# Optimization experiments

Hardware: AMD Instinct MI355X
Metric: run time of the kernel (lower is better)

## Reference

```python
import jax, jax.numpy as jnp
import numpy as np

B, T, D, C, L, H = 8192, 128, 1, 1, 1, 64


def _mlp(x, w1, b1, w2, b2):
    # Linear -> Softplus -> Linear
    return jax.nn.softplus(x @ w1 + b1) @ w2 + b2


def setup_inputs() -> dict:
    key = jax.random.key(0)
    ks = jax.random.split(key, 32)
    s = 0.1

    def w(k, shape):
        return jax.random.normal(k, shape, jnp.float32) * s

    p = {}
    p["xs"] = jax.random.normal(ks[0], (T, B, D), jnp.float32)
    p["ts"] = jnp.arange(T, dtype=jnp.float32)
    p["noise_std"] = jnp.float32(5.0)
    p["eps0"] = jax.random.normal(ks[1], (B, L), jnp.float32)
    p["dW_std"] = jax.random.normal(ks[2], (T - 1, B, L), jnp.float32)
    # encoder: data -> hidden -> context
    p["ew1"] = w(ks[3], (D, H)); p["eb1"] = w(ks[4], (H,))
    p["ew2"] = w(ks[5], (H, C)); p["eb2"] = w(ks[6], (C,))
    # qz0_net: context -> 2*latent
    p["qw"] = w(ks[7], (C, 2 * L)); p["qb"] = w(ks[8], (2 * L,))
    # f_net: latent+context -> hidden -> latent
    p["fw1"] = w(ks[9], (L + C, H)); p["fb1"] = w(ks[10], (H,))
    p["fw2"] = w(ks[11], (H, L)); p["fb2"] = w(ks[12], (L,))
    # h_net: latent -> hidden -> latent
    p["hw1"] = w(ks[13], (L, H)); p["hb1"] = w(ks[14], (H,))
    p["hw2"] = w(ks[15], (H, L)); p["hb2"] = w(ks[16], (L,))
    # g_nets: L independent 1 -> hidden -> 1 -> sigmoid nets, stacked on leading L axis
    p["gw1"] = w(ks[17], (L, H)); p["gb1"] = w(ks[18], (L, H))
    p["gw2"] = w(ks[19], (L, H)); p["gb2"] = w(ks[20], (L,))
    # projector: latent -> hidden -> data
    p["pw1"] = w(ks[21], (L, H)); p["pb1"] = w(ks[22], (H,))
    p["pw2"] = w(ks[23], (H, D)); p["pb2"] = w(ks[24], (D,))
    p["pz0_mean"] = jnp.zeros((1, L), jnp.float32)
    p["pz0_logstd"] = jnp.zeros((1, L), jnp.float32)
    return p


def reference(xs, ts, noise_std, eps0, dW_std,
              ew1, eb1, ew2, eb2, qw, qb,
              fw1, fb1, fw2, fb2, hw1, hb1, hw2, hb2,
              gw1, gb1, gw2, gb2, pw1, pb1, pw2, pb2,
              pz0_mean, pz0_logstd):
    Tn = ts.shape[0]
    # ctx = flip(encoder(flip(xs)))  (encoder is pointwise in time)
    ctx = jnp.flip(_mlp(jnp.flip(xs, axis=0), ew1, eb1, ew2, eb2), axis=0)  # [T,B,C]
    qz = ctx[0] @ qw + qb
    qm, qls = jnp.split(qz, 2, axis=1)  # [B,L] each
    z0 = qm + jnp.exp(qls) * eps0

    def g_fn(z):  # per-coordinate diagonal diffusion nets
        hid = jax.nn.softplus(z[:, :, None] * gw1[None] + gb1[None])  # [B,L,H]
        return jax.nn.sigmoid(jnp.einsum('blh,lh->bl', hid, gw2) + gb2)

    def step(z, inp):
        k, dwk = inp
        t = ts[k]
        dt = ts[k + 1] - ts[k]
        idx = jnp.minimum(jnp.searchsorted(ts, t, side='right'), Tn - 1)
        c = jnp.take(ctx, idx, axis=0)  # [B,C]
        fv = _mlp(jnp.concatenate([z, c], axis=1), fw1, fb1, fw2, fb2)
        hv = _mlp(z, hw1, hb1, hw2, hb2)
        gv = g_fn(z)
        u = (fv - hv) / gv
        lr = 0.5 * jnp.sum(u * u, axis=1) * dt  # logqp path increment [B]
        z_next = z + fv * dt + gv * dwk * jnp.sqrt(dt)  # Euler-Maruyama
        return z_next, (z_next, lr)

    _, (ztail, log_ratio) = jax.lax.scan(step, z0, (jnp.arange(Tn - 1), dW_std))
    zs = jnp.concatenate([z0[None], ztail], axis=0)  # [T,B,L]
    _xs = _mlp(zs, pw1, pb1, pw2, pb2)  # [T,B,D]
    lp = -0.5 * ((xs - _xs) / noise_std) ** 2 - jnp.log(noise_std) - 0.5 * jnp.log(2 * jnp.pi)
    log_pxs = lp.sum(axis=(0, 2)).mean()
    kl = (pz0_logstd - qls) + (jnp.exp(2 * qls) + (qm - pz0_mean) ** 2) / (2 * jnp.exp(2 * pz0_logstd)) - 0.5
    logqp0 = kl.sum(axis=1).mean()
    logqp_path = log_ratio.sum(axis=0).mean()
    return (log_pxs, logqp0 + logqp_path)
```

## Files before the change

kernel.cpp:

```cpp
#include <hip/hip_runtime.h>
#include <math.h>


#define B_SZ 8192
#define T_SZ 128
#define NBLK 32

#define NT1 2049
#define NT2 1025
#define NEE 1024
#define NENT (NT1 + NT2 + NEE)

#define MT_FLOATS (8 * (NT1 + NT2))
#define ET2G_OFF  MT_FLOATS
#define TABG_FLOATS (MT_FLOATS + 2048)
#define T2_BASE4 (2 * NT1)

#define NXI 1024
#define XSF 64.0f
#define XOF 512.0f

#if __has_builtin(__builtin_amdgcn_rcpf)
#define RCPF(x) __builtin_amdgcn_rcpf(x)
#else
#define RCPF(x) (1.0f / (x))
#endif
#if __has_builtin(__builtin_amdgcn_sqrtf)
#define SQRTF(x) __builtin_amdgcn_sqrtf(x)
#else
#define SQRTF(x) sqrtf(x)
#endif

__device__ __forceinline__ float sp_precise(float a) {
  return fmaxf(a, 0.0f) + log1pf(expf(-fabsf(a)));
}
__device__ __forceinline__ float wsum64(float v) {
  #pragma unroll
  for (int m = 1; m <= 32; m <<= 1) v += __shfl_xor(v, m);
  return v;
}

__global__ __launch_bounds__(256) void build_tabs(
    const float* __restrict__ ew1, const float* __restrict__ eb1,
    const float* __restrict__ ew2, const float* __restrict__ eb2,
    const float* __restrict__ fw1, const float* __restrict__ fb1,
    const float* __restrict__ fw2, const float* __restrict__ fb2,
    const float* __restrict__ hw1, const float* __restrict__ hb1,
    const float* __restrict__ hw2, const float* __restrict__ hb2,
    const float* __restrict__ gw1, const float* __restrict__ gb1,
    const float* __restrict__ gw2, const float* __restrict__ gb2,
    const float* __restrict__ pw1, const float* __restrict__ pb1,
    const float* __restrict__ pw2, const float* __restrict__ pb2,
    float* __restrict__ tabs, int* __restrict__ ctr)
{
  const int gtid = blockIdx.x * 256 + threadIdx.x;
  if (gtid == 0) *ctr = 0;
  const int ent  = gtid >> 6;
  const int lane = threadIdx.x & 63;
  if (ent >= NENT) return;

  if (ent < NT1 + NT2) {
    const bool t1 = ent < NT1;
    const int  i  = t1 ? ent : (ent - NT1);
    const float z = t1 ? (-128.0f + (float)i * 0.125f)
                       : (-8192.0f + (float)i * 16.0f);
    const int base4 = (t1 ? 0 : T2_BASE4) + 2 * i;

    const float az = fmaf(z, fw1[lane], fb1[lane]);
    const float wc = fw1[64 + lane], w2 = fw2[lane];
    float s0 = sp_precise(fmaf(-3.0f, wc, az)) * w2;
    float s1 = sp_precise(fmaf(-1.0f, wc, az)) * w2;
    float s2 = sp_precise(fmaf( 1.0f, wc, az)) * w2;
    float s3 = sp_precise(fmaf( 3.0f, wc, az)) * w2;
    float sh = sp_precise(fmaf(z, hw1[lane], hb1[lane])) * hw2[lane];
    float sg = sp_precise(fmaf(z, gw1[lane], gb1[lane])) * gw2[lane];
    float sp = sp_precise(fmaf(z, pw1[lane], pb1[lane])) * pw2[lane];
    s0 = wsum64(s0); s1 = wsum64(s1); s2 = wsum64(s2); s3 = wsum64(s3);
    sh = wsum64(sh); sg = wsum64(sg); sp = wsum64(sp);
    if (lane == 0) {
      const float fb = fb2[0];
      ((float4*)tabs)[base4]     = make_float4(s0 + fb, s1 + fb, s2 + fb, s3 + fb);
      ((float4*)tabs)[base4 + 1] = make_float4(
          sh + hb2[0],
          1.0f / (1.0f + expf(-(sg + gb2[0]))),
          sp + pb2[0], 0.0f);
    }
  } else {
    const int i = ent - (NT1 + NT2);
    const float x0 = -8.0f + (float)i * (1.0f / 64.0f);
    const float x1 = x0 + (1.0f / 64.0f);
    const float w = ew1[lane], bb = eb1[lane], w2 = ew2[lane];
    float s0 = sp_precise(fmaf(x0, w, bb)) * w2;
    float s1 = sp_precise(fmaf(x1, w, bb)) * w2;
    s0 = wsum64(s0); s1 = wsum64(s1);
    if (lane == 0) {
      const float eb = eb2[0];
      ((float2*)(tabs + ET2G_OFF))[i] = make_float2(s0 + eb, s1 + eb);
    }
  }
}

__global__ __launch_bounds__(256) void ctx_pre(
    const float* __restrict__ xs, const float* __restrict__ tabs,
    float* __restrict__ ctx)
{
  const int i = blockIdx.x * 256 + threadIdx.x;
  const float2* et2 = (const float2*)(tabs + ET2G_OFF);
  const float s = fmaf(xs[i], XSF, XOF);
  const float sc = fminf(fmaxf(s, 0.0f), (float)(NXI - 1));
  const int ii = (int)sc;
  const float fr = s - (float)ii;
  const float2 e = et2[ii];
  ctx[i] = fmaf(fr, e.y - e.x, e.x);
}

__global__ __launch_bounds__(256) void sde_scan(
    const float* __restrict__ xs, const float* __restrict__ ts,
    const float* __restrict__ noise_std, const float* __restrict__ eps0,
    const float* __restrict__ dW, const float* __restrict__ ctx,
    const float* __restrict__ qw,  const float* __restrict__ qb,
    const float* __restrict__ fw1, const float* __restrict__ fb1,
    const float* __restrict__ fw2, const float* __restrict__ fb2,
    const float* __restrict__ hw1, const float* __restrict__ hb1,
    const float* __restrict__ hw2, const float* __restrict__ hb2,
    const float* __restrict__ gw1, const float* __restrict__ gb1,
    const float* __restrict__ gw2, const float* __restrict__ gb2,
    const float* __restrict__ pw1, const float* __restrict__ pb1,
    const float* __restrict__ pw2, const float* __restrict__ pb2,
    const float* __restrict__ pz0_mean, const float* __restrict__ pz0_logstd,
    const float* __restrict__ tabsrc,
    int* __restrict__ ctr, float* __restrict__ partA, float* __restrict__ partB,
    float* __restrict__ out)
{
  __shared__ __align__(16) float tab[MT_FLOATS];
  __shared__ float la[256], lb[256];
  __shared__ int lastflag;

  const int tid = threadIdx.x;
  const int b   = blockIdx.x * 256 + tid;

  {
    const float4* s4 = (const float4*)tabsrc;
    float4* d4 = (float4*)tab;
    for (int i = tid; i < MT_FLOATS / 4; i += 256) d4[i] = s4[i];
  }
  __syncthreads();

  const float4* tab4 = (const float4*)tab;

  const float fb2s = fb2[0], hb2s = hb2[0], gb2s = gb2[0], pb2s = pb2[0];
  const float qw0 = qw[0], qw1 = qw[1], qb0 = qb[0], qb1 = qb[1];
  const float ns = noise_std[0];
  const float inv_ns = 1.0f / ns;
  const float nh_i2 = -0.5f * inv_ns * inv_ns;
  const float pm = pz0_mean[0], pls = pz0_logstd[0];

  auto lagr = [&](float c) {
    const float c2 = c * c;
    const float p1 = c2 - 1.0f, p3 = c2 - 9.0f;
    return make_float4(p1 * (c - 3.0f) * (-1.0f / 48.0f),
                       p3 * (c - 1.0f) * ( 1.0f / 16.0f),
                       p3 * (c + 1.0f) * (-1.0f / 16.0f),
                       p1 * (c + 3.0f) * ( 1.0f / 48.0f));
  };
  auto hgp_exact = [&](float z, float& hv, float& gv, float& pv) {
    float sh = 0.f, sg = 0.f, sp = 0.f;
    for (int j = 0; j < 64; ++j) {
      sh = fmaf(sp_precise(fmaf(z, hw1[j], hb1[j])), hw2[j], sh);
      sg = fmaf(sp_precise(fmaf(z, gw1[j], gb1[j])), gw2[j], sg);
      sp = fmaf(sp_precise(fmaf(z, pw1[j], pb1[j])), pw2[j], sp);
    }
    hv = sh + hb2s;
    gv = 1.0f / (1.0f + expf(-(sg + gb2s)));
    pv = sp + pb2s;
  };
  auto f_exact = [&](float z, float c) {
    float s = 0.f;
    for (int j = 0; j < 64; ++j)
      s = fmaf(sp_precise(fmaf(z, fw1[j], fmaf(c, fw1[64 + j], fb1[j]))), fw2[j], s);
    return s + fb2s;
  };

  auto zidx = [&](float z, int& base4, float& frac, bool& inr) {
    const float s1 = fmaf(z, 8.0f, 1024.0f);
    const float s2 = fmaf(z, 0.0625f, 512.0f);
    const bool t1 = (s1 >= 0.0f) && (s1 <= 2048.0f);
    const bool t2 = (s2 >= 0.0f) && (s2 <= 1024.0f);
    inr = t1 || t2;
    const float sf = t1 ? s1 : fminf(fmaxf(s2, 0.0f), 1024.0f);
    const int fi = min((int)sf, t1 ? (NT1 - 2) : (NT2 - 2));
    base4 = (t1 ? 0 : T2_BASE4) + 2 * fi;
    frac = sf - (float)fi;
  };

  const float x0 = xs[b];
  float x1 = xs[B_SZ + b];
  float x2 = xs[2 * B_SZ + b];
  const float c0v = ctx[b];
  float c_cur = ctx[B_SZ + b];
  float c_nxt = ctx[2 * B_SZ + b];
  const float qm  = fmaf(c0v, qw0, qb0);
  const float qls = fmaf(c0v, qw1, qb1);
  float z = fmaf(__expf(qls), eps0[b], qm);
  const float dqm = qm - pm;
  const float kl = (pls - qls)
                 + (__expf(2.0f * qls) + dqm * dqm) * (0.5f * __expf(-2.0f * pls))
                 - 0.5f;

  bool zin; int zb4; float zfr;
  float4 q0a, q0b, q1a, q1b;
  float hv, gv, pv;
  zidx(z, zb4, zfr, zin);
  q0a = tab4[zb4]; q0b = tab4[zb4 + 1]; q1a = tab4[zb4 + 2]; q1b = tab4[zb4 + 3];
  if (zin) {
    hv = fmaf(zfr, q1b.x - q0b.x, q0b.x);
    gv = fmaf(zfr, q1b.y - q0b.y, q0b.y);
    pv = fmaf(zfr, q1b.z - q0b.z, q0b.z);
  } else {
    hgp_exact(z, hv, gv, pv);
  }
  float lp_sum; { const float d = x0 - pv; lp_sum = nh_i2 * d * d; }
  float lr_sum = 0.0f;
  float dw_cur = dW[b];
  float dw_n1  = dW[B_SZ + b];
  float4 L = lagr(c_cur);
  bool cin = fabsf(c_cur) <= 3.0f;

  for (int k = 0; k < T_SZ - 1; ++k) {
    const int   i3    = (k + 3 < T_SZ) ? (k + 3) : (T_SZ - 1);
    const float x3    = xs[i3 * B_SZ + b];
    const float c3    = ctx[i3 * B_SZ + b];
    const float dw_n2 = (k + 2 < T_SZ - 1) ? dW[(k + 2) * B_SZ + b] : 0.0f;
    const float dt    = ts[k + 1] - ts[k];
    const float sq    = SQRTF(dt);

    float fv;
    if (zin && cin) {
      const float n0 = fmaf(zfr, q1a.x - q0a.x, q0a.x);
      const float n1 = fmaf(zfr, q1a.y - q0a.y, q0a.y);
      const float n2 = fmaf(zfr, q1a.z - q0a.z, q0a.z);
      const float n3 = fmaf(zfr, q1a.w - q0a.w, q0a.w);
      fv = n0 * L.x + n1 * L.y + n2 * L.z + n3 * L.w;
    } else {
      fv = f_exact(z, c_cur);
    }

    const float gvs = fmaxf(gv, 1e-6f);
    const float uu = (fv - hv) * RCPF(gvs);
    lr_sum = fmaf((0.5f * dt) * uu, uu, lr_sum);
    z = fmaf(gvs * dw_cur, sq, fmaf(fv, dt, z));

    zidx(z, zb4, zfr, zin);
    q0a = tab4[zb4]; q0b = tab4[zb4 + 1]; q1a = tab4[zb4 + 2]; q1b = tab4[zb4 + 3];
    if (zin) {
      hv = fmaf(zfr, q1b.x - q0b.x, q0b.x);
      gv = fmaf(zfr, q1b.y - q0b.y, q0b.y);
      pv = fmaf(zfr, q1b.z - q0b.z, q0b.z);
    } else {
      hgp_exact(z, hv, gv, pv);
    }

    const float d = x1 - pv;
    lp_sum = fmaf(nh_i2 * d, d, lp_sum);

    c_cur = c_nxt; L = lagr(c_cur); cin = fabsf(c_cur) <= 3.0f;
    c_nxt = c3;
    x1 = x2; x2 = x3;
    dw_cur = dw_n1; dw_n1 = dw_n2;
  }

  la[tid] = lp_sum; lb[tid] = kl + lr_sum;
  __syncthreads();
  for (int s = 128; s > 0; s >>= 1) {
    if (tid < s) { la[tid] += la[tid + s]; lb[tid] += lb[tid + s]; }
    __syncthreads();
  }
  if (tid == 0) {
    partA[blockIdx.x] = la[0]; partB[blockIdx.x] = lb[0];
    __threadfence();
    lastflag = (atomicAdd(ctr, 1) == NBLK - 1) ? 1 : 0;
  }
  __syncthreads();
  if (lastflag) {
    __threadfence();
    la[tid] = (tid < NBLK) ? partA[tid] : 0.0f;
    lb[tid] = (tid < NBLK) ? partB[tid] : 0.0f;
    __syncthreads();
    for (int s = 128; s > 0; s >>= 1) {
      if (tid < s) { la[tid] += la[tid + s]; lb[tid] += lb[tid + s]; }
      __syncthreads();
    }
    if (tid == 0) {
      out[0] = la[0] / (float)B_SZ
             + (float)T_SZ * (-__logf(ns) - 0.9189385332046727f);
      out[1] = lb[0] / (float)B_SZ;
    }
  }
}

extern "C" void kernel_launch(void* const* d_in, const int* in_sizes, int n_in,
                              void* d_out, int out_size, void* d_ws, size_t ws_size,
                              hipStream_t stream) {
  const float* xs        = (const float*)d_in[0];
  const float* ts        = (const float*)d_in[1];
  const float* noise_std = (const float*)d_in[2];
  const float* eps0      = (const float*)d_in[3];
  const float* dW        = (const float*)d_in[4];
  const float* ew1 = (const float*)d_in[5];
  const float* eb1 = (const float*)d_in[6];
  const float* ew2 = (const float*)d_in[7];
  const float* eb2 = (const float*)d_in[8];
  const float* qw  = (const float*)d_in[9];
  const float* qb  = (const float*)d_in[10];
  const float* fw1 = (const float*)d_in[11];
  const float* fb1 = (const float*)d_in[12];
  const float* fw2 = (const float*)d_in[13];
  const float* fb2 = (const float*)d_in[14];
  const float* hw1 = (const float*)d_in[15];
  const float* hb1 = (const float*)d_in[16];
  const float* hw2 = (const float*)d_in[17];
  const float* hb2 = (const float*)d_in[18];
  const float* gw1 = (const float*)d_in[19];
  const float* gb1 = (const float*)d_in[20];
  const float* gw2 = (const float*)d_in[21];
  const float* gb2 = (const float*)d_in[22];
  const float* pw1 = (const float*)d_in[23];
  const float* pb1 = (const float*)d_in[24];
  const float* pw2 = (const float*)d_in[25];
  const float* pb2 = (const float*)d_in[26];
  const float* pz0_mean   = (const float*)d_in[27];
  const float* pz0_logstd = (const float*)d_in[28];
  float* out = (float*)d_out;

  float* tabs  = (float*)d_ws;
  int*   ctr   = (int*)(tabs + TABG_FLOATS);
  float* partA = tabs + TABG_FLOATS + 4;
  float* partB = partA + NBLK;
  float* ctxb  = tabs + TABG_FLOATS + 72;

  build_tabs<<<(NENT * 64 + 255) / 256, 256, 0, stream>>>(
      ew1, eb1, ew2, eb2, fw1, fb1, fw2, fb2,
      hw1, hb1, hw2, hb2, gw1, gb1, gw2, gb2,
      pw1, pb1, pw2, pb2, tabs, ctr);

  ctx_pre<<<(T_SZ * B_SZ) / 256, 256, 0, stream>>>(xs, tabs, ctxb);

  sde_scan<<<NBLK, 256, 0, stream>>>(
      xs, ts, noise_std, eps0, dW, ctxb, qw, qb,
      fw1, fb1, fw2, fb2, hw1, hb1, hw2, hb2,
      gw1, gb1, gw2, gb2, pw1, pb1, pw2, pb2,
      pz0_mean, pz0_logstd, tabs, ctr, partA, partB, out);
}
```

Measured before the change: 73.85 us.

## Shrink z lookup table, pad entries to three float4s, deepen prefetch to four steps

Halves the resolution of the fine z table (step 0.25 instead of 0.125) so it holds half as many entries, and gives each entry a stride of three float4 instead of two, with the third slot zero-filled. The time loop is manually unrolled by four and uses a four-deep rotating register buffer for xs, ctx and dW loads, which hides global load latency across more steps. The coarser table lowers interpolation accuracy for f/h/g/p, and the padded stride adds table memory and raises the chance of gather cache misses.

```diff
diff --git a/kernel.cpp b/kernel.cpp
--- a/kernel.cpp
+++ b/kernel.cpp
@@ -6,15 +6,16 @@
 #define T_SZ 128
 #define NBLK 32
 
-#define NT1 2049
+#define NT1 1025
 #define NT2 1025
 #define NEE 1024
 #define NENT (NT1 + NT2 + NEE)
 
-#define MT_FLOATS (8 * (NT1 + NT2))
+#define ENT_F4 3
+#define MT_FLOATS (4 * ENT_F4 * (NT1 + NT2))
+#define T2_BASE4 (ENT_F4 * NT1)
 #define ET2G_OFF  MT_FLOATS
 #define TABG_FLOATS (MT_FLOATS + 2048)
-#define T2_BASE4 (2 * NT1)
 
 #define NXI 1024
 #define XSF 64.0f
@@ -62,9 +63,9 @@
   if (ent < NT1 + NT2) {
     const bool t1 = ent < NT1;
     const int  i  = t1 ? ent : (ent - NT1);
-    const float z = t1 ? (-128.0f + (float)i * 0.125f)
+    const float z = t1 ? (-128.0f + (float)i * 0.25f)
                        : (-8192.0f + (float)i * 16.0f);
-    const int base4 = (t1 ? 0 : T2_BASE4) + 2 * i;
+    const int base4 = (t1 ? 0 : T2_BASE4) + ENT_F4 * i;
 
     const float az = fmaf(z, fw1[lane], fb1[lane]);
     const float wc = fw1[64 + lane], w2 = fw2[lane];
@@ -84,6 +85,7 @@
           sh + hb2[0],
           1.0f / (1.0f + expf(-(sg + gb2[0]))),
           sp + pb2[0], 0.0f);
+      ((float4*)tabs)[base4 + 2] = make_float4(0.f, 0.f, 0.f, 0.f);
     }
   } else {
     const int i = ent - (NT1 + NT2);
@@ -163,42 +165,37 @@
                        p3 * (c + 1.0f) * (-1.0f / 16.0f),
                        p1 * (c + 3.0f) * ( 1.0f / 48.0f));
   };
-  auto hgp_exact = [&](float z, float& hv, float& gv, float& pv) {
+  auto hgp_exact = [&](float z_, float& hv_, float& gv_, float& pv_) {
     float sh = 0.f, sg = 0.f, sp = 0.f;
     for (int j = 0; j < 64; ++j) {
-      sh = fmaf(sp_precise(fmaf(z, hw1[j], hb1[j])), hw2[j], sh);
-      sg = fmaf(sp_precise(fmaf(z, gw1[j], gb1[j])), gw2[j], sg);
-      sp = fmaf(sp_precise(fmaf(z, pw1[j], pb1[j])), pw2[j], sp);
-    }
-    hv = sh + hb2s;
-    gv = 1.0f / (1.0f + expf(-(sg + gb2s)));
-    pv = sp + pb2s;
+      sh = fmaf(sp_precise(fmaf(z_, hw1[j], hb1[j])), hw2[j], sh);
+      sg = fmaf(sp_precise(fmaf(z_, gw1[j], gb1[j])), gw2[j], sg);
+      sp = fmaf(sp_precise(fmaf(z_, pw1[j], pb1[j])), pw2[j], sp);
+    }
+    hv_ = sh + hb2s;
+    gv_ = 1.0f / (1.0f + expf(-(sg + gb2s)));
+    pv_ = sp + pb2s;
   };
-  auto f_exact = [&](float z, float c) {
+  auto f_exact = [&](float z_, float c_) {
     float s = 0.f;
     for (int j = 0; j < 64; ++j)
-      s = fmaf(sp_precise(fmaf(z, fw1[j], fmaf(c, fw1[64 + j], fb1[j]))), fw2[j], s);
+      s = fmaf(sp_precise(fmaf(z_, fw1[j], fmaf(c_, fw1[64 + j], fb1[j]))), fw2[j], s);
     return s + fb2s;
   };
-
-  auto zidx = [&](float z, int& base4, float& frac, bool& inr) {
-    const float s1 = fmaf(z, 8.0f, 1024.0f);
-    const float s2 = fmaf(z, 0.0625f, 512.0f);
-    const bool t1 = (s1 >= 0.0f) && (s1 <= 2048.0f);
+  auto zidx = [&](float z_, int& base4_, float& frac_, bool& inr_) {
+    const float s1 = fmaf(z_, 4.0f, 512.0f);
+    const float s2 = fmaf(z_, 0.0625f, 512.0f);
+    const bool t1 = (s1 >= 0.0f) && (s1 <= 1024.0f);
     const bool t2 = (s2 >= 0.0f) && (s2 <= 1024.0f);
-    inr = t1 || t2;
+    inr_ = t1 || t2;
     const float sf = t1 ? s1 : fminf(fmaxf(s2, 0.0f), 1024.0f);
-    const int fi = min((int)sf, t1 ? (NT1 - 2) : (NT2 - 2));
-    base4 = (t1 ? 0 : T2_BASE4) + 2 * fi;
-    frac = sf - (float)fi;
+    const int fi = min((int)sf, 1023);
+    base4_ = (t1 ? 0 : T2_BASE4) + ENT_F4 * fi;
+    frac_ = sf - (float)fi;
   };
 
   const float x0 = xs[b];
-  float x1 = xs[B_SZ + b];
-  float x2 = xs[2 * B_SZ + b];
   const float c0v = ctx[b];
-  float c_cur = ctx[B_SZ + b];
-  float c_nxt = ctx[2 * B_SZ + b];
   const float qm  = fmaf(c0v, qw0, qb0);
   const float qls = fmaf(c0v, qw1, qb1);
   float z = fmaf(__expf(qls), eps0[b], qm);
@@ -207,11 +204,17 @@
                  + (__expf(2.0f * qls) + dqm * dqm) * (0.5f * __expf(-2.0f * pls))
                  - 0.5f;
 
+  float xbuf0 = xs[1 * B_SZ + b], cbuf0 = ctx[1 * B_SZ + b], wbuf0 = dW[0 * B_SZ + b];
+  float xbuf1 = xs[2 * B_SZ + b], cbuf1 = ctx[2 * B_SZ + b], wbuf1 = dW[1 * B_SZ + b];
+  float xbuf2 = xs[3 * B_SZ + b], cbuf2 = ctx[3 * B_SZ + b], wbuf2 = dW[2 * B_SZ + b];
+  float xbuf3 = xs[4 * B_SZ + b], cbuf3 = ctx[4 * B_SZ + b], wbuf3 = dW[3 * B_SZ + b];
+
   bool zin; int zb4; float zfr;
   float4 q0a, q0b, q1a, q1b;
   float hv, gv, pv;
   zidx(z, zb4, zfr, zin);
-  q0a = tab4[zb4]; q0b = tab4[zb4 + 1]; q1a = tab4[zb4 + 2]; q1b = tab4[zb4 + 3];
+  q0a = tab4[zb4]; q0b = tab4[zb4 + 1];
+  q1a = tab4[zb4 + ENT_F4]; q1b = tab4[zb4 + ENT_F4 + 1];
   if (zin) {
     hv = fmaf(zfr, q1b.x - q0b.x, q0b.x);
     gv = fmaf(zfr, q1b.y - q0b.y, q0b.y);
@@ -221,53 +224,53 @@
   }
   float lp_sum; { const float d = x0 - pv; lp_sum = nh_i2 * d * d; }
   float lr_sum = 0.0f;
-  float dw_cur = dW[b];
-  float dw_n1  = dW[B_SZ + b];
-  float4 L = lagr(c_cur);
-  bool cin = fabsf(c_cur) <= 3.0f;
-
-  for (int k = 0; k < T_SZ - 1; ++k) {
-    const int   i3    = (k + 3 < T_SZ) ? (k + 3) : (T_SZ - 1);
-    const float x3    = xs[i3 * B_SZ + b];
-    const float c3    = ctx[i3 * B_SZ + b];
-    const float dw_n2 = (k + 2 < T_SZ - 1) ? dW[(k + 2) * B_SZ + b] : 0.0f;
-    const float dt    = ts[k + 1] - ts[k];
-    const float sq    = SQRTF(dt);
-
-    float fv;
-    if (zin && cin) {
-      const float n0 = fmaf(zfr, q1a.x - q0a.x, q0a.x);
-      const float n1 = fmaf(zfr, q1a.y - q0a.y, q0a.y);
-      const float n2 = fmaf(zfr, q1a.z - q0a.z, q0a.z);
-      const float n3 = fmaf(zfr, q1a.w - q0a.w, q0a.w);
-      fv = n0 * L.x + n1 * L.y + n2 * L.z + n3 * L.w;
-    } else {
-      fv = f_exact(z, c_cur);
-    }
-
-    const float gvs = fmaxf(gv, 1e-6f);
-    const float uu = (fv - hv) * RCPF(gvs);
-    lr_sum = fmaf((0.5f * dt) * uu, uu, lr_sum);
-    z = fmaf(gvs * dw_cur, sq, fmaf(fv, dt, z));
-
-    zidx(z, zb4, zfr, zin);
-    q0a = tab4[zb4]; q0b = tab4[zb4 + 1]; q1a = tab4[zb4 + 2]; q1b = tab4[zb4 + 3];
-    if (zin) {
-      hv = fmaf(zfr, q1b.x - q0b.x, q0b.x);
-      gv = fmaf(zfr, q1b.y - q0b.y, q0b.y);
-      pv = fmaf(zfr, q1b.z - q0b.z, q0b.z);
-    } else {
-      hgp_exact(z, hv, gv, pv);
-    }
-
-    const float d = x1 - pv;
-    lp_sum = fmaf(nh_i2 * d, d, lp_sum);
-
-    c_cur = c_nxt; L = lagr(c_cur); cin = fabsf(c_cur) <= 3.0f;
-    c_nxt = c3;
-    x1 = x2; x2 = x3;
-    dw_cur = dw_n1; dw_n1 = dw_n2;
-  }
+
+#define STEP(K, J) { \
+    const float dt = ts[(K) + 1] - ts[(K)]; \
+    const float sq = SQRTF(dt); \
+    const float cc = cbuf##J; \
+    const float4 L = lagr(cc); \
+    const bool cin = fabsf(cc) <= 3.0f; \
+    float fv; \
+    if (zin && cin) { \
+      const float n0 = fmaf(zfr, q1a.x - q0a.x, q0a.x); \
+      const float n1 = fmaf(zfr, q1a.y - q0a.y, q0a.y); \
+      const float n2 = fmaf(zfr, q1a.z - q0a.z, q0a.z); \
+      const float n3 = fmaf(zfr, q1a.w - q0a.w, q0a.w); \
+      fv = n0 * L.x + n1 * L.y + n2 * L.z + n3 * L.w; \
+    } else { \
+      fv = f_exact(z, cc); \
+    } \
+    const float gvs = fmaxf(gv, 1e-6f); \
+    const float uu = (fv - hv) * RCPF(gvs); \
+    lr_sum = fmaf((0.5f * dt) * uu, uu, lr_sum); \
+    z = fmaf(gvs * wbuf##J, sq, fmaf(fv, dt, z)); \
+    zidx(z, zb4, zfr, zin); \
+    q0a = tab4[zb4]; q0b = tab4[zb4 + 1]; \
+    q1a = tab4[zb4 + ENT_F4]; q1b = tab4[zb4 + ENT_F4 + 1]; \
+     \
+    const int kk_ = (K) + 4; \
+    const int ix_ = ((kk_ + 1 < T_SZ) ? kk_ + 1 : T_SZ - 1) * B_SZ + b; \
+    const float xb_n = xs[ix_]; \
+    const float cb_n = ctx[ix_]; \
+    const float wb_n = (kk_ < T_SZ - 1) ? dW[kk_ * B_SZ + b] : 0.0f; \
+    if (zin) { \
+      hv = fmaf(zfr, q1b.x - q0b.x, q0b.x); \
+      gv = fmaf(zfr, q1b.y - q0b.y, q0b.y); \
+      pv = fmaf(zfr, q1b.z - q0b.z, q0b.z); \
+    } else { \
+      hgp_exact(z, hv, gv, pv); \
+    } \
+    const float d_ = xbuf##J - pv; \
+    lp_sum = fmaf(nh_i2 * d_, d_, lp_sum); \
+    xbuf##J = xb_n; cbuf##J = cb_n; wbuf##J = wb_n; \
+  }
+
+  for (int k = 0; k < 124; k += 4) {
+    STEP(k, 0); STEP(k + 1, 1); STEP(k + 2, 2); STEP(k + 3, 3);
+  }
+  STEP(124, 0); STEP(125, 1); STEP(126, 2);
+#undef STEP
 
   la[tid] = lp_sum; lb[tid] = kl + lr_sum;
   __syncthreads();
```

After: 61.91 us. 16.2% less time.
